# Kernel tuning notes

Hardware: AMD Instinct MI355X
Metric: run time of the kernel (lower is better)

The kernel has to match this reference:

```python
import jax, jax.numpy as jnp
import numpy as np

NU, NI = 100000, 50000          # users, items
N = NU + NI                      # total nodes
E0 = 1200000                     # directed user->item interactions
B = 100000                       # query (user,item) pairs
D = 64                           # embedding_dim
H1, H2, H3 = 128, 128, 64        # hidden_dims


def setup_inputs() -> dict:
    key = jax.random.key(0)
    ks = jax.random.split(key, 20)
    # bipartite edges, made symmetric (as create_graph does)
    u = jax.random.randint(ks[0], (E0,), 0, NU, dtype=jnp.int32)
    it = jax.random.randint(ks[1], (E0,), NU, N, dtype=jnp.int32)
    src = jnp.concatenate([u, it])   # [2*E0]
    dst = jnp.concatenate([it, u])   # [2*E0]
    user_idx = jax.random.randint(ks[2], (B,), 0, NU, dtype=jnp.int32)
    item_idx = jax.random.randint(ks[3], (B,), 0, NI, dtype=jnp.int32)

    def w(k, shape, fan_in):
        return jax.random.normal(k, shape, jnp.float32) * (1.0 / np.sqrt(fan_in))

    return {
        "user_table": jax.random.normal(ks[4], (NU, D), jnp.float32),
        "item_table": jax.random.normal(ks[5], (NI, D), jnp.float32),
        "W1": w(ks[6], (D, H1), D),   "b1": jnp.zeros((H1,), jnp.float32),
        "W2": w(ks[7], (H1, H2), H1), "b2": jnp.zeros((H2,), jnp.float32),
        "W3": w(ks[8], (H2, H3), H2), "b3": jnp.zeros((H3,), jnp.float32),
        "P1": w(ks[9], (2 * H3, 64), 2 * H3), "pb1": jnp.zeros((64,), jnp.float32),
        "P2": w(ks[10], (64, 32), 64),        "pb2": jnp.zeros((32,), jnp.float32),
        "P3": w(ks[11], (32, 1), 32),         "pb3": jnp.zeros((1,), jnp.float32),
        "src": src, "dst": dst,
        "user_idx": user_idx, "item_idx": item_idx,
    }


def _gconv(x, src, dst, deg_rsqrt, W, b):
    # DGL GraphConv, norm='both': D^{-1/2} A D^{-1/2} X W + b
    h = x * deg_rsqrt[:, None]                              # [N, d]
    m = jax.ops.segment_sum(h[src], dst, num_segments=N)    # gather-scatter over edges
    return (m * deg_rsqrt[:, None]) @ W + b


def reference(user_table, item_table, W1, b1, W2, b2, W3, b3,
              P1, pb1, P2, pb2, P3, pb3, src, dst, user_idx, item_idx):
    # symmetric graph -> in-degree == out-degree
    deg = jax.ops.segment_sum(jnp.ones_like(dst, jnp.float32), dst, num_segments=N)
    deg_rsqrt = jax.lax.rsqrt(jnp.maximum(deg, 1.0))

    x = jnp.concatenate([user_table, item_table], axis=0)   # [N, D]
    x = jax.nn.relu(_gconv(x, src, dst, deg_rsqrt, W1, b1))
    x = jax.nn.relu(_gconv(x, src, dst, deg_rsqrt, W2, b2))
    x = _gconv(x, src, dst, deg_rsqrt, W3, b3)               # [N, H3]

    u = x[user_idx]                                          # [B, H3]
    v = x[NU + item_idx]                                     # [B, H3]
    z = jnp.concatenate([u, v], axis=1)                      # [B, 2*H3]
    z = jax.nn.relu(z @ P1 + pb1)
    z = jax.nn.relu(z @ P2 + pb2)
    return jax.nn.sigmoid(z @ P3 + pb3)                      # [B, 1]
```

## Files before the change

kernel.cpp:

```cpp
#include <hip/hip_runtime.h>
#include <hip/hip_bf16.h>


typedef unsigned short u16;
typedef unsigned int   u32;
typedef __attribute__((ext_vector_type(8))) short short8;
typedef __attribute__((ext_vector_type(4))) float f32x4;

__device__ __forceinline__ float b2f(u16 u){
  union { u32 i; float f; } c; c.i = ((u32)u) << 16; return c.f;
}
__device__ __forceinline__ u16 f2b(float f){
  union { float f; u32 i; } c; c.f = f;
  u32 x = c.i;
  u32 r = x + 0x7FFFu + ((x >> 16) & 1u);
  return (u16)(r >> 16);
}

__device__ __forceinline__ void acc8(uint4 u, float* a){
  a[0] += b2f((u16)(u.x & 0xffff)); a[1] += b2f((u16)(u.x >> 16));
  a[2] += b2f((u16)(u.y & 0xffff)); a[3] += b2f((u16)(u.y >> 16));
  a[4] += b2f((u16)(u.z & 0xffff)); a[5] += b2f((u16)(u.z >> 16));
  a[6] += b2f((u16)(u.w & 0xffff)); a[7] += b2f((u16)(u.w >> 16));
}


__global__ __launch_bounds__(256) void k_histK(const int* __restrict__ dst, int ne, int K,
                                               u32* __restrict__ bhist){
  extern __shared__ u32 sh[];
  int t = threadIdx.x;
  for (int i = t; i < K; i += 256) sh[i] = 0;
  __syncthreads();
  for (int i = blockIdx.x*256 + t; i < ne; i += gridDim.x*256)
    atomicAdd(&sh[dst[i] >> 8], 1u);
  __syncthreads();
  int rot = (int)((blockIdx.x * 73u) % (u32)K);
  for (int jj = t; jj < K; jj += 256){
    int i = jj + rot; if (i >= K) i -= K;
    u32 v = sh[i];
    if (v) atomicAdd(&bhist[i], v);
  }
}

__global__ __launch_bounds__(256) void k_scanK(const u32* __restrict__ bhist, int K,
                                               u32* __restrict__ bbase, u32* __restrict__ gcur){
  __shared__ u32 s[256];
  int t = threadIdx.x;
  int items = (K + 255) / 256;
  u32 local[16];
  int s0 = t * items;
  u32 sum = 0;
  for (int j = 0; j < items; j++){
    int idx = s0 + j;
    u32 v = (idx < K) ? bhist[idx] : 0;
    local[j] = v; sum += v;
  }
  s[t] = sum; __syncthreads();
  for (int off = 1; off < 256; off <<= 1){
    u32 add = (t >= off) ? s[t-off] : 0;
    __syncthreads();
    s[t] += add;
    __syncthreads();
  }
  u32 run = s[t] - sum;
  for (int j = 0; j < items; j++){
    int idx = s0 + j;
    if (idx < K){ bbase[idx] = run; gcur[idx] = run; }
    run += local[j];
  }
  if (t == 255) bbase[K] = s[255];
}

__global__ __launch_bounds__(256) void k_scatterR(const int* __restrict__ src, const int* __restrict__ dst,
                                                  int ne, int K, u32* __restrict__ gcur,
                                                  u32* __restrict__ ebuf){
  extern __shared__ u32 cnt[];
  int t = threadIdx.x;
  int e0 = blockIdx.x * 4096;
  for (int i = t; i < K; i += 256) cnt[i] = 0;
  __syncthreads();
#pragma unroll
  for (int j = 0; j < 16; j++){
    int e = e0 + j*256 + t;
    if (e < ne) atomicAdd(&cnt[dst[e] >> 8], 1u);
  }
  __syncthreads();
  int rot = (int)((blockIdx.x * 73u) % (u32)K);
  for (int jj = t; jj < K; jj += 256){
    int i = jj + rot; if (i >= K) i -= K;
    u32 c = cnt[i];
    if (c) cnt[i] = atomicAdd(&gcur[i], c);
  }
  __syncthreads();
#pragma unroll
  for (int j = 0; j < 16; j++){
    int e = e0 + j*256 + t;
    if (e < ne){
      int d = dst[e];
      u32 p = atomicAdd(&cnt[d >> 8], 1u);
      ebuf[p] = ((u32)(d & 255) << 18) | (u32)src[e];
    }
  }
}

__global__ __launch_bounds__(256) void k_csr(const u32* __restrict__ ebuf, const u32* __restrict__ bbase,
                                             int n, int ne, int* __restrict__ row_ptr,
                                             float* __restrict__ r, int* __restrict__ col){
  __shared__ u32 cnt[256];
  __shared__ u32 pfx[256];
  __shared__ u32 cur[256];
  int b = blockIdx.x, t = threadIdx.x;
  u32 bb = bbase[b], be = bbase[b+1];
  int nbase = b << 8;
  int nn = n - nbase; if (nn > 256) nn = 256;
  cnt[t] = 0;
  __syncthreads();
  for (u32 e = bb + t; e < be; e += 256)
    atomicAdd(&cnt[ebuf[e] >> 18], 1u);
  __syncthreads();
  pfx[t] = cnt[t];
  __syncthreads();
  for (int off = 1; off < 256; off <<= 1){
    u32 add = (t >= off) ? pfx[t-off] : 0;
    __syncthreads();
    pfx[t] += add;
    __syncthreads();
  }
  u32 excl = pfx[t] - cnt[t];
  cur[t] = bb + excl;
  if (t < nn){
    row_ptr[nbase + t] = (int)(bb + excl);
    r[nbase + t] = rsqrtf(fmaxf((float)cnt[t], 1.0f));
  }
  __syncthreads();
  for (u32 e = bb + t; e < be; e += 256){
    u32 v = ebuf[e];
    u32 p = atomicAdd(&cur[v >> 18], 1u);
    col[p] = (int)(v & 0x3FFFFu);
  }
  if (b == 0 && t == 0) row_ptr[n] = ne;
}

__global__ __launch_bounds__(256) void k_cvtW(const float* __restrict__ a0, const float* __restrict__ a1,
    const float* __restrict__ a2, const float* __restrict__ a3, const float* __restrict__ a4,
    int n0, int n1, int n2, int n3, int n4, u16* __restrict__ out){
  int i = blockIdx.x*256 + threadIdx.x;
  int idx = i;
  const float* s;
  if (idx < n0){ s = a0; }
  else { idx -= n0;
    if (idx < n1){ s = a1; }
    else { idx -= n1;
      if (idx < n2){ s = a2; }
      else { idx -= n2;
        if (idx < n3){ s = a3; }
        else { idx -= n3;
          if (idx >= n4) return;
          s = a4;
        }
      }
    }
  }
  out[i] = f2b(s[idx]);
}

__global__ __launch_bounds__(256) void k_scale0(const float* __restrict__ ut, const float* __restrict__ it,
    const float* __restrict__ r, u16* __restrict__ x0, int n, int nu){
  int i = blockIdx.x*256 + threadIdx.x;
  int base = i*4;
  if (base < n*64){
    int node = base >> 6;
    float rv = r[node];
    const float* srcp = (node < nu) ? (ut + (size_t)node*64) : (it + (size_t)(node-nu)*64);
    float4 v = *(const float4*)(srcp + (base & 63));
    ushort4 o;
    o.x = f2b(v.x*rv); o.y = f2b(v.y*rv); o.z = f2b(v.z*rv); o.w = f2b(v.w*rv);
    *(ushort4*)(x0 + base) = o;
  }
}

template<int D, bool BIAS>
__global__ __launch_bounds__(256) void k_agg(const u16* __restrict__ x, const float* __restrict__ r,
    const int* __restrict__ row_ptr, const int* __restrict__ col,
    const float* __restrict__ bias, u16* __restrict__ out, int n){
  constexpr int G = D/8;
  constexpr int E = 64/G;
  int wid = (blockIdx.x*256 + threadIdx.x) >> 6;
  int lane = threadIdx.x & 63;
  if (wid >= n) return;
  int gidx = lane / G;
  int l    = lane % G;
  int beg = row_ptr[wid], end = row_ptr[wid+1];
  float a[8] = {0.f,0.f,0.f,0.f,0.f,0.f,0.f,0.f};
  int e = beg + gidx;
  for (; e + E < end; e += 2*E){
    int s0 = col[e];
    int s1 = col[e+E];
    uint4 u0 = *(const uint4*)(x + (size_t)s0*D + l*8);
    uint4 u1 = *(const uint4*)(x + (size_t)s1*D + l*8);
    acc8(u0, a);
    acc8(u1, a);
  }
  if (e < end){
    int s = col[e];
    acc8(*(const uint4*)(x + (size_t)s*D + l*8), a);
  }
#pragma unroll
  for (int off = G; off < 64; off <<= 1){
#pragma unroll
    for (int i = 0; i < 8; i++) a[i] += __shfl_xor(a[i], off);
  }
  if (gidx == 0){
    float rn = r[wid];
    float v[8];
#pragma unroll
    for (int i = 0; i < 8; i++){
      float y = a[i] * rn;
      if constexpr (BIAS) y += bias[l*8 + i];
      v[i] = y;
    }
    uint4 o;
    o.x = (u32)f2b(v[0]) | ((u32)f2b(v[1]) << 16);
    o.y = (u32)f2b(v[2]) | ((u32)f2b(v[3]) << 16);
    o.z = (u32)f2b(v[4]) | ((u32)f2b(v[5]) << 16);
    o.w = (u32)f2b(v[6]) | ((u32)f2b(v[7]) << 16);
    *(uint4*)(out + (size_t)wid*D + l*8) = o;
  }
}

template<int K_, int OUT, bool BIAS, bool RELU, bool SCALE, bool GATHER, bool DOTEP>
__global__ __launch_bounds__(256) void k_mgemm(
    const u16* __restrict__ A, const u16* __restrict__ Wb, const float* __restrict__ bias,
    const float* __restrict__ rr, u16* __restrict__ C, int nrows, int nu,
    const int* __restrict__ uidx, const int* __restrict__ vidx,
    const float* __restrict__ P3, const float* __restrict__ pb3, float* __restrict__ outp)
{
  constexpr int KP = K_ + 8;
  constexpr int NT = OUT / 16;
  constexpr int KS = K_ / 32;
  __shared__ u16 Wt[OUT * KP];
  const int t = threadIdx.x;

  for (int i = t; i < (K_*OUT)/2; i += 256){
    int g = i*2;
    int k = g / OUT, n = g % OUT;
    u32 v = *(const u32*)(Wb + (size_t)k*OUT + n);
    Wt[n*KP + k]     = (u16)(v & 0xffff);
    Wt[(n+1)*KP + k] = (u16)(v >> 16);
  }
  __syncthreads();

  const int wave = t >> 6, lane = t & 63;
  const int quad = lane >> 4, m16 = lane & 15;
  const int rowb = blockIdx.x*128 + wave*32;

  const short8 zz = {0,0,0,0,0,0,0,0};
  short8 afr[2][KS];
#pragma unroll
  for (int mt = 0; mt < 2; mt++){
    int row = rowb + mt*16 + m16;
    bool ok = row < nrows;
#pragma unroll
    for (int ks = 0; ks < KS; ks++){
      int k = ks*32 + quad*8;
      if (!ok){ afr[mt][ks] = zz; continue; }
      if constexpr (GATHER){
        int node, kk;
        if (k < 64){ node = uidx[row];      kk = k; }
        else       { node = nu + vidx[row]; kk = k - 64; }
        afr[mt][ks] = *(const short8*)(A + (size_t)node*64 + kk);
      } else {
        afr[mt][ks] = *(const short8*)(A + (size_t)row*K_ + k);
      }
    }
  }

  f32x4 acc[2][NT];
#pragma unroll
  for (int mt = 0; mt < 2; mt++)
#pragma unroll
    for (int nt = 0; nt < NT; nt++) acc[mt][nt] = (f32x4){0.f,0.f,0.f,0.f};

#pragma unroll
  for (int nt = 0; nt < NT; nt++){
#pragma unroll
    for (int ks = 0; ks < KS; ks++){
      short8 b = *(const short8*)(Wt + (size_t)(nt*16 + m16)*KP + ks*32 + quad*8);
      acc[0][nt] = __builtin_amdgcn_mfma_f32_16x16x32_bf16(afr[0][ks], b, acc[0][nt], 0, 0, 0);
      acc[1][nt] = __builtin_amdgcn_mfma_f32_16x16x32_bf16(afr[1][ks], b, acc[1][nt], 0, 0, 0);
    }
  }

  if constexpr (!DOTEP){
    float bv[NT];
#pragma unroll
    for (int nt = 0; nt < NT; nt++){
      if constexpr (BIAS) bv[nt] = bias[nt*16 + m16]; else bv[nt] = 0.f;
    }
#pragma unroll
    for (int mt = 0; mt < 2; mt++){
      int row0 = rowb + mt*16 + quad*4;
#pragma unroll
      for (int reg = 0; reg < 4; reg++){
        int row = row0 + reg;
        if (row >= nrows) continue;
        float rs = 1.f;
        if constexpr (SCALE) rs = rr[row];
#pragma unroll
        for (int nt = 0; nt < NT; nt++){
          float v = acc[mt][nt][reg];
          if constexpr (BIAS) v += bv[nt];
          if constexpr (RELU) v = fmaxf(v, 0.f);
          if constexpr (SCALE) v *= rs;
          C[(size_t)row*OUT + nt*16 + m16] = f2b(v);
        }
      }
    }
  } else {
    float b0 = bias[m16], b1v = bias[16 + m16];
    float p0 = P3[m16],   p1 = P3[16 + m16];
    float pb = pb3[0];
#pragma unroll
    for (int mt = 0; mt < 2; mt++){
      float v4[4];
#pragma unroll
      for (int reg = 0; reg < 4; reg++){
        float part = fmaxf(acc[mt][0][reg] + b0, 0.f) * p0
                   + fmaxf(acc[mt][1][reg] + b1v, 0.f) * p1;
        part += __shfl_xor(part, 1);
        part += __shfl_xor(part, 2);
        part += __shfl_xor(part, 4);
        part += __shfl_xor(part, 8);
        v4[reg] = 1.f / (1.f + __expf(-(part + pb)));
      }
      if (m16 == 0){
        int row0 = rowb + mt*16 + quad*4;
        if (row0 + 3 < nrows){
          *(float4*)(outp + row0) = make_float4(v4[0], v4[1], v4[2], v4[3]);
        } else {
#pragma unroll
          for (int reg = 0; reg < 4; reg++)
            if (row0 + reg < nrows) outp[row0 + reg] = v4[reg];
        }
      }
    }
  }
}


extern "C" void kernel_launch(void* const* d_in, const int* in_sizes, int n_in,
                              void* d_out, int out_size, void* d_ws, size_t ws_size,
                              hipStream_t stream){
  const float* ut  = (const float*)d_in[0];
  const float* it  = (const float*)d_in[1];
  const float* W1  = (const float*)d_in[2];
  const float* b1  = (const float*)d_in[3];
  const float* W2  = (const float*)d_in[4];
  const float* b2  = (const float*)d_in[5];
  const float* W3  = (const float*)d_in[6];
  const float* b3  = (const float*)d_in[7];
  const float* P1  = (const float*)d_in[8];
  const float* pb1 = (const float*)d_in[9];
  const float* P2  = (const float*)d_in[10];
  const float* pb2 = (const float*)d_in[11];
  const float* P3  = (const float*)d_in[12];
  const float* pb3 = (const float*)d_in[13];
  const int* src  = (const int*)d_in[14];
  const int* dst  = (const int*)d_in[15];
  const int* uidx = (const int*)d_in[16];
  const int* vidx = (const int*)d_in[17];

  const int NU = in_sizes[0] / 64;
  const int NI = in_sizes[1] / 64;
  const int N  = NU + NI;
  const int NE = in_sizes[14];
  const int B  = in_sizes[16];
  const int K  = (N + 255) >> 8;

  char* w = (char*)d_ws;
  auto alloc = [&](size_t bytes)->void*{
    void* p = (void*)w;
    w += (bytes + 255) & ~(size_t)255;
    return p;
  };
  float* r       = (float*)alloc((size_t)N*4);
  int*   row_ptr = (int*)  alloc((size_t)(N+1)*4);
  u32*   bhist   = (u32*)  alloc((size_t)K*4);
  u32*   bbase   = (u32*)  alloc((size_t)(K+1)*4);
  u32*   gcur    = (u32*)  alloc((size_t)K*4);
  int*   col     = (int*)  alloc((size_t)NE*4);
  u16*   Wall    = (u16*)  alloc((size_t)(64*128 + 128*128 + 128*64 + 128*64 + 64*32)*2);
  char*  bufE    = (char*) alloc((size_t)N*64*2 > (size_t)NE*4 ? (size_t)N*64*2 : (size_t)NE*4);
  char*  bufF    = (char*) alloc((size_t)N*128*2);
  u16*   bufC    = (u16*)  alloc((size_t)N*128*2);
  u16*   bufD    = (u16*)  alloc((size_t)N*64*2);
  if ((size_t)(w - (char*)d_ws) > ws_size) return;

  u16* wb1  = Wall;
  u16* wb2  = wb1 + 64*128;
  u16* wb3  = wb2 + 128*128;
  u16* pb1w = wb3 + 128*64;
  u16* pb2w = pb1w + 128*64;
  const int NW = 64*128 + 128*128 + 128*64 + 128*64 + 64*32;

  u32* ebuf = (u32*)bufE;

  hipMemsetAsync(bhist, 0, (size_t)K*4, stream);

  int g;
  k_cvtW   <<<(NW + 255)/256, 256, 0, stream>>>(W1, W2, W3, P1, P2,
              64*128, 128*128, 128*64, 128*64, 64*32, Wall);
  k_histK  <<<128, 256, (size_t)K*4, stream>>>(dst, NE, K, bhist);
  k_scanK  <<<1, 256, 0, stream>>>(bhist, K, bbase, gcur);
  g = (NE + 4095)/4096;
  k_scatterR<<<g, 256, (size_t)K*4, stream>>>(src, dst, NE, K, gcur, ebuf);
  k_csr    <<<K, 256, 0, stream>>>(ebuf, bbase, N, NE, row_ptr, r, col);

  const int ga  = (N + 3)/4;
  const int gN  = (N + 127)/128;
  const int gB  = (B + 127)/128;

  u16* x0 = bufD;
  g = (N*64/4 + 255)/256; k_scale0<<<g,256,0,stream>>>(ut, it, r, x0, N, NU);

  u16* m1 = (u16*)bufE;
  k_agg<64,false><<<ga,256,0,stream>>>(x0, r, row_ptr, col, nullptr, m1, N);
  u16* h1 = bufC;
  k_mgemm<64,128,true,true,true,false,false><<<gN,256,0,stream>>>(
      m1, wb1, b1, r, h1, N, NU, nullptr, nullptr, nullptr, nullptr, nullptr);

  u16* m2 = (u16*)bufF;
  k_agg<128,false><<<ga,256,0,stream>>>(h1, r, row_ptr, col, nullptr, m2, N);
  u16* h2 = bufC;
  k_mgemm<128,128,true,true,true,false,false><<<gN,256,0,stream>>>(
      m2, wb2, b2, r, h2, N, NU, nullptr, nullptr, nullptr, nullptr, nullptr);

  u16* g3 = bufD;
  k_mgemm<128,64,false,false,false,false,false><<<gN,256,0,stream>>>(
      h2, wb3, nullptr, nullptr, g3, N, NU, nullptr, nullptr, nullptr, nullptr, nullptr);

  u16* x3 = (u16*)bufE;
  k_agg<64,true><<<ga,256,0,stream>>>(g3, r, row_ptr, col, b3, x3, N);

  u16* A1 = (u16*)bufF;
  k_mgemm<128,64,true,true,false,true,false><<<gB,256,0,stream>>>(
      x3, pb1w, pb1, nullptr, A1, B, NU, uidx, vidx, nullptr, nullptr, nullptr);

  k_mgemm<64,32,true,true,false,false,true><<<gB,256,0,stream>>>(
      A1, pb2w, pb2, nullptr, nullptr, B, 0, nullptr, nullptr, P3, pb3, (float*)d_out);
}
```

Measured before the change: 488.5 us.

## Fuse weight conversion, input scaling and MLP head; pre-transpose weights

Weight conversion to bf16 moves into the histogram kernel and now writes transposed weights, so the GEMM kernels read B fragments straight from global memory instead of staging a transposed copy in shared memory. The input scaling by degree is folded into the CSR kernel, and the two prediction-head GEMMs are merged into one kernel that keeps the intermediate in shared memory. This removes three launches, one shared-memory transpose per GEMM block and a global round trip of the hidden activations. In exchange, weight fragments are fetched repeatedly from global/L2 instead of shared memory.

```diff
diff --git a/kernel.cpp b/kernel.cpp
--- a/kernel.cpp
+++ b/kernel.cpp
@@ -24,11 +24,24 @@
   a[6] += b2f((u16)(u.w & 0xffff)); a[7] += b2f((u16)(u.w >> 16));
 }
 
+#define NWT 43008
+
 
 __global__ __launch_bounds__(256) void k_histK(const int* __restrict__ dst, int ne, int K,
-                                               u32* __restrict__ bhist){
+    u32* __restrict__ bhist,
+    const float* __restrict__ W1, const float* __restrict__ W2, const float* __restrict__ W3,
+    const float* __restrict__ P1, const float* __restrict__ P2, u16* __restrict__ WT){
   extern __shared__ u32 sh[];
   int t = threadIdx.x;
+  for (int i = blockIdx.x*256 + t; i < NWT; i += gridDim.x*256){
+    float v;
+    if (i < 8192)      { int j=i;        v = W1[(j%64)*128 + j/64];   }
+    else if (i < 24576){ int j=i-8192;   v = W2[(j%128)*128 + j/128]; }
+    else if (i < 32768){ int j=i-24576;  v = W3[(j%128)*64 + j/128];  }
+    else if (i < 40960){ int j=i-32768;  v = P1[(j%128)*64 + j/128];  }
+    else               { int j=i-40960;  v = P2[(j%64)*32 + j/64];    }
+    WT[i] = f2b(v);
+  }
   for (int i = t; i < K; i += 256) sh[i] = 0;
   __syncthreads();
   for (int i = blockIdx.x*256 + t; i < ne; i += gridDim.x*256)
@@ -105,10 +118,13 @@
 
 __global__ __launch_bounds__(256) void k_csr(const u32* __restrict__ ebuf, const u32* __restrict__ bbase,
                                              int n, int ne, int* __restrict__ row_ptr,
-                                             float* __restrict__ r, int* __restrict__ col){
+                                             float* __restrict__ r, int* __restrict__ col,
+                                             const float* __restrict__ ut, const float* __restrict__ it,
+                                             int nu, u16* __restrict__ x0){
   __shared__ u32 cnt[256];
   __shared__ u32 pfx[256];
   __shared__ u32 cur[256];
+  __shared__ float rsh[256];
   int b = blockIdx.x, t = threadIdx.x;
   u32 bb = bbase[b], be = bbase[b+1];
   int nbase = b << 8;
@@ -129,8 +145,10 @@
   u32 excl = pfx[t] - cnt[t];
   cur[t] = bb + excl;
   if (t < nn){
+    float rv = rsqrtf(fmaxf((float)cnt[t], 1.0f));
     row_ptr[nbase + t] = (int)(bb + excl);
-    r[nbase + t] = rsqrtf(fmaxf((float)cnt[t], 1.0f));
+    r[nbase + t] = rv;
+    rsh[t] = rv;
   }
   __syncthreads();
   for (u32 e = bb + t; e < be; e += 256){
@@ -139,43 +157,17 @@
     col[p] = (int)(v & 0x3FFFFu);
   }
   if (b == 0 && t == 0) row_ptr[n] = ne;
-}
-
-__global__ __launch_bounds__(256) void k_cvtW(const float* __restrict__ a0, const float* __restrict__ a1,
-    const float* __restrict__ a2, const float* __restrict__ a3, const float* __restrict__ a4,
-    int n0, int n1, int n2, int n3, int n4, u16* __restrict__ out){
-  int i = blockIdx.x*256 + threadIdx.x;
-  int idx = i;
-  const float* s;
-  if (idx < n0){ s = a0; }
-  else { idx -= n0;
-    if (idx < n1){ s = a1; }
-    else { idx -= n1;
-      if (idx < n2){ s = a2; }
-      else { idx -= n2;
-        if (idx < n3){ s = a3; }
-        else { idx -= n3;
-          if (idx >= n4) return;
-          s = a4;
-        }
-      }
-    }
-  }
-  out[i] = f2b(s[idx]);
-}
-
-__global__ __launch_bounds__(256) void k_scale0(const float* __restrict__ ut, const float* __restrict__ it,
-    const float* __restrict__ r, u16* __restrict__ x0, int n, int nu){
-  int i = blockIdx.x*256 + threadIdx.x;
-  int base = i*4;
-  if (base < n*64){
-    int node = base >> 6;
-    float rv = r[node];
-    const float* srcp = (node < nu) ? (ut + (size_t)node*64) : (it + (size_t)(node-nu)*64);
-    float4 v = *(const float4*)(srcp + (base & 63));
+  for (int i = t; i < nn*16; i += 256){
+    int ln = i >> 4;
+    int node = nbase + ln;
+    int c4 = (i & 15) << 2;
+    float rv = rsh[ln];
+    const float* srcp = (node < nu) ? (ut + (size_t)node*64 + c4)
+                                    : (it + (size_t)(node-nu)*64 + c4);
+    float4 v = *(const float4*)srcp;
     ushort4 o;
     o.x = f2b(v.x*rv); o.y = f2b(v.y*rv); o.z = f2b(v.z*rv); o.w = f2b(v.w*rv);
-    *(ushort4*)(x0 + base) = o;
+    *(ushort4*)(x0 + (size_t)node*64 + c4) = o;
   }
 }
 
@@ -228,28 +220,14 @@
   }
 }
 
-template<int K_, int OUT, bool BIAS, bool RELU, bool SCALE, bool GATHER, bool DOTEP>
+template<int K_, int OUT, bool BIAS, bool RELU, bool SCALE>
 __global__ __launch_bounds__(256) void k_mgemm(
-    const u16* __restrict__ A, const u16* __restrict__ Wb, const float* __restrict__ bias,
-    const float* __restrict__ rr, u16* __restrict__ C, int nrows, int nu,
-    const int* __restrict__ uidx, const int* __restrict__ vidx,
-    const float* __restrict__ P3, const float* __restrict__ pb3, float* __restrict__ outp)
+    const u16* __restrict__ A, const u16* __restrict__ WT, const float* __restrict__ bias,
+    const float* __restrict__ rr, u16* __restrict__ C, int nrows)
 {
-  constexpr int KP = K_ + 8;
   constexpr int NT = OUT / 16;
   constexpr int KS = K_ / 32;
-  __shared__ u16 Wt[OUT * KP];
   const int t = threadIdx.x;
-
-  for (int i = t; i < (K_*OUT)/2; i += 256){
-    int g = i*2;
-    int k = g / OUT, n = g % OUT;
-    u32 v = *(const u32*)(Wb + (size_t)k*OUT + n);
-    Wt[n*KP + k]     = (u16)(v & 0xffff);
-    Wt[(n+1)*KP + k] = (u16)(v >> 16);
-  }
-  __syncthreads();
-
   const int wave = t >> 6, lane = t & 63;
   const int quad = lane >> 4, m16 = lane & 15;
   const int rowb = blockIdx.x*128 + wave*32;
@@ -262,86 +240,158 @@
     bool ok = row < nrows;
 #pragma unroll
     for (int ks = 0; ks < KS; ks++){
+      afr[mt][ks] = ok ? *(const short8*)(A + (size_t)row*K_ + ks*32 + quad*8) : zz;
+    }
+  }
+
+  f32x4 acc[2][NT];
+#pragma unroll
+  for (int mt = 0; mt < 2; mt++)
+#pragma unroll
+    for (int nt = 0; nt < NT; nt++) acc[mt][nt] = (f32x4){0.f,0.f,0.f,0.f};
+
+#pragma unroll
+  for (int nt = 0; nt < NT; nt++){
+#pragma unroll
+    for (int ks = 0; ks < KS; ks++){
+      short8 b = *(const short8*)(WT + (size_t)(nt*16 + m16)*K_ + ks*32 + quad*8);
+      acc[0][nt] = __builtin_amdgcn_mfma_f32_16x16x32_bf16(afr[0][ks], b, acc[0][nt], 0, 0, 0);
+      acc[1][nt] = __builtin_amdgcn_mfma_f32_16x16x32_bf16(afr[1][ks], b, acc[1][nt], 0, 0, 0);
+    }
+  }
+
+  float bv[NT];
+#pragma unroll
+  for (int nt = 0; nt < NT; nt++){
+    if constexpr (BIAS) bv[nt] = bias[nt*16 + m16]; else bv[nt] = 0.f;
+  }
+#pragma unroll
+  for (int mt = 0; mt < 2; mt++){
+    int row0 = rowb + mt*16 + quad*4;
+#pragma unroll
+    for (int reg = 0; reg < 4; reg++){
+      int row = row0 + reg;
+      if (row >= nrows) continue;
+      float rs = 1.f;
+      if constexpr (SCALE) rs = rr[row];
+#pragma unroll
+      for (int nt = 0; nt < NT; nt++){
+        float v = acc[mt][nt][reg];
+        if constexpr (BIAS) v += bv[nt];
+        if constexpr (RELU) v = fmaxf(v, 0.f);
+        if constexpr (SCALE) v *= rs;
+        C[(size_t)row*OUT + nt*16 + m16] = f2b(v);
+      }
+    }
+  }
+}
+
+__global__ __launch_bounds__(256) void k_mlp(
+    const u16* __restrict__ x3, const u16* __restrict__ WT4, const float* __restrict__ pb1v,
+    const u16* __restrict__ WT5, const float* __restrict__ pb2v,
+    const float* __restrict__ P3, const float* __restrict__ pb3,
+    const int* __restrict__ uidx, const int* __restrict__ vidx,
+    int B, int nu, float* __restrict__ outp)
+{
+  __shared__ u16 a1[128*72];
+  const int t = threadIdx.x;
+  const int wave = t >> 6, lane = t & 63;
+  const int quad = lane >> 4, m16 = lane & 15;
+  const int rowb = blockIdx.x*128 + wave*32;
+
+  const short8 zz = {0,0,0,0,0,0,0,0};
+  short8 afr[2][4];
+#pragma unroll
+  for (int mt = 0; mt < 2; mt++){
+    int row = rowb + mt*16 + m16;
+    bool ok = row < B;
+#pragma unroll
+    for (int ks = 0; ks < 4; ks++){
       int k = ks*32 + quad*8;
       if (!ok){ afr[mt][ks] = zz; continue; }
-      if constexpr (GATHER){
-        int node, kk;
-        if (k < 64){ node = uidx[row];      kk = k; }
-        else       { node = nu + vidx[row]; kk = k - 64; }
-        afr[mt][ks] = *(const short8*)(A + (size_t)node*64 + kk);
-      } else {
-        afr[mt][ks] = *(const short8*)(A + (size_t)row*K_ + k);
-      }
-    }
-  }
-
-  f32x4 acc[2][NT];
+      int node, kk;
+      if (k < 64){ node = uidx[row];      kk = k; }
+      else       { node = nu + vidx[row]; kk = k - 64; }
+      afr[mt][ks] = *(const short8*)(x3 + (size_t)node*64 + kk);
+    }
+  }
+  f32x4 acc[2][4];
 #pragma unroll
   for (int mt = 0; mt < 2; mt++)
 #pragma unroll
-    for (int nt = 0; nt < NT; nt++) acc[mt][nt] = (f32x4){0.f,0.f,0.f,0.f};
-
-#pragma unroll
-  for (int nt = 0; nt < NT; nt++){
-#pragma unroll
-    for (int ks = 0; ks < KS; ks++){
-      short8 b = *(const short8*)(Wt + (size_t)(nt*16 + m16)*KP + ks*32 + quad*8);
+    for (int nt = 0; nt < 4; nt++) acc[mt][nt] = (f32x4){0.f,0.f,0.f,0.f};
+#pragma unroll
+  for (int nt = 0; nt < 4; nt++){
+#pragma unroll
+    for (int ks = 0; ks < 4; ks++){
+      short8 b = *(const short8*)(WT4 + (size_t)(nt*16 + m16)*128 + ks*32 + quad*8);
       acc[0][nt] = __builtin_amdgcn_mfma_f32_16x16x32_bf16(afr[0][ks], b, acc[0][nt], 0, 0, 0);
       acc[1][nt] = __builtin_amdgcn_mfma_f32_16x16x32_bf16(afr[1][ks], b, acc[1][nt], 0, 0, 0);
     }
   }
-
-  if constexpr (!DOTEP){
-    float bv[NT];
-#pragma unroll
-    for (int nt = 0; nt < NT; nt++){
-      if constexpr (BIAS) bv[nt] = bias[nt*16 + m16]; else bv[nt] = 0.f;
-    }
-#pragma unroll
-    for (int mt = 0; mt < 2; mt++){
+  float pb1s[4];
+#pragma unroll
+  for (int nt = 0; nt < 4; nt++) pb1s[nt] = pb1v[nt*16 + m16];
+#pragma unroll
+  for (int mt = 0; mt < 2; mt++){
+    int rl0 = wave*32 + mt*16 + quad*4;
+#pragma unroll
+    for (int reg = 0; reg < 4; reg++){
+#pragma unroll
+      for (int nt = 0; nt < 4; nt++){
+        float v = fmaxf(acc[mt][nt][reg] + pb1s[nt], 0.f);
+        a1[(rl0 + reg)*72 + nt*16 + m16] = f2b(v);
+      }
+    }
+  }
+  __syncthreads();
+
+  short8 af2[2][2];
+#pragma unroll
+  for (int mt = 0; mt < 2; mt++){
+    int rl = wave*32 + mt*16 + m16;
+#pragma unroll
+    for (int ks = 0; ks < 2; ks++)
+      af2[mt][ks] = *(const short8*)(a1 + rl*72 + ks*32 + quad*8);
+  }
+  f32x4 acc2[2][2];
+#pragma unroll
+  for (int mt = 0; mt < 2; mt++)
+#pragma unroll
+    for (int nt = 0; nt < 2; nt++) acc2[mt][nt] = (f32x4){0.f,0.f,0.f,0.f};
+#pragma unroll
+  for (int nt = 0; nt < 2; nt++){
+#pragma unroll
+    for (int ks = 0; ks < 2; ks++){
+      short8 b = *(const short8*)(WT5 + (size_t)(nt*16 + m16)*64 + ks*32 + quad*8);
+      acc2[0][nt] = __builtin_amdgcn_mfma_f32_16x16x32_bf16(af2[0][ks], b, acc2[0][nt], 0, 0, 0);
+      acc2[1][nt] = __builtin_amdgcn_mfma_f32_16x16x32_bf16(af2[1][ks], b, acc2[1][nt], 0, 0, 0);
+    }
+  }
+  float b0 = pb2v[m16], b1v = pb2v[16 + m16];
+  float p0 = P3[m16],   p1 = P3[16 + m16];
+  float pb = pb3[0];
+#pragma unroll
+  for (int mt = 0; mt < 2; mt++){
+    float v4[4];
+#pragma unroll
+    for (int reg = 0; reg < 4; reg++){
+      float part = fmaxf(acc2[mt][0][reg] + b0, 0.f) * p0
+                 + fmaxf(acc2[mt][1][reg] + b1v, 0.f) * p1;
+      part += __shfl_xor(part, 1);
+      part += __shfl_xor(part, 2);
+      part += __shfl_xor(part, 4);
+      part += __shfl_xor(part, 8);
+      v4[reg] = 1.f / (1.f + __expf(-(part + pb)));
+    }
+    if (m16 == 0){
       int row0 = rowb + mt*16 + quad*4;
-#pragma unroll
-      for (int reg = 0; reg < 4; reg++){
-        int row = row0 + reg;
-        if (row >= nrows) continue;
-        float rs = 1.f;
-        if constexpr (SCALE) rs = rr[row];
-#pragma unroll
-        for (int nt = 0; nt < NT; nt++){
-          float v = acc[mt][nt][reg];
-          if constexpr (BIAS) v += bv[nt];
-          if constexpr (RELU) v = fmaxf(v, 0.f);
-          if constexpr (SCALE) v *= rs;
-          C[(size_t)row*OUT + nt*16 + m16] = f2b(v);
-        }
-      }
-    }
-  } else {
-    float b0 = bias[m16], b1v = bias[16 + m16];
-    float p0 = P3[m16],   p1 = P3[16 + m16];
-    float pb = pb3[0];
-#pragma unroll
-    for (int mt = 0; mt < 2; mt++){
-      float v4[4];
-#pragma unroll
-      for (int reg = 0; reg < 4; reg++){
-        float part = fmaxf(acc[mt][0][reg] + b0, 0.f) * p0
-                   + fmaxf(acc[mt][1][reg] + b1v, 0.f) * p1;
-        part += __shfl_xor(part, 1);
-        part += __shfl_xor(part, 2);
-        part += __shfl_xor(part, 4);
-        part += __shfl_xor(part, 8);
-        v4[reg] = 1.f / (1.f + __expf(-(part + pb)));
-      }
-      if (m16 == 0){
-        int row0 = rowb + mt*16 + quad*4;
-        if (row0 + 3 < nrows){
-          *(float4*)(outp + row0) = make_float4(v4[0], v4[1], v4[2], v4[3]);
-        } else {
-#pragma unroll
-          for (int reg = 0; reg < 4; reg++)
-            if (row0 + reg < nrows) outp[row0 + reg] = v4[reg];
-        }
+      if (row0 + 3 < B){
+        *(float4*)(outp + row0) = make_float4(v4[0], v4[1], v4[2], v4[3]);
+      } else {
+#pragma unroll
+        for (int reg = 0; reg < 4; reg++)
+          if (row0 + reg < B) outp[row0 + reg] = v4[reg];
       }
     }
   }
@@ -389,63 +439,50 @@
   u32*   bbase   = (u32*)  alloc((size_t)(K+1)*4);
   u32*   gcur    = (u32*)  alloc((size_t)K*4);
   int*   col     = (int*)  alloc((size_t)NE*4);
-  u16*   Wall    = (u16*)  alloc((size_t)(64*128 + 128*128 + 128*64 + 128*64 + 64*32)*2);
+  u16*   Wall    = (u16*)  alloc((size_t)NWT*2);
   char*  bufE    = (char*) alloc((size_t)N*64*2 > (size_t)NE*4 ? (size_t)N*64*2 : (size_t)NE*4);
   char*  bufF    = (char*) alloc((size_t)N*128*2);
   u16*   bufC    = (u16*)  alloc((size_t)N*128*2);
   u16*   bufD    = (u16*)  alloc((size_t)N*64*2);
   if ((size_t)(w - (char*)d_ws) > ws_size) return;
 
-  u16* wb1  = Wall;
-  u16* wb2  = wb1 + 64*128;
-  u16* wb3  = wb2 + 128*128;
-  u16* pb1w = wb3 + 128*64;
-  u16* pb2w = pb1w + 128*64;
-  const int NW = 64*128 + 128*128 + 128*64 + 128*64 + 64*32;
+  u16* WT1 = Wall;
+  u16* WT2 = Wall + 8192;
+  u16* WT3 = Wall + 24576;
+  u16* WT4 = Wall + 32768;
+  u16* WT5 = Wall + 40960;
 
   u32* ebuf = (u32*)bufE;
+  u16* x0   = bufD;
 
   hipMemsetAsync(bhist, 0, (size_t)K*4, stream);
 
   int g;
-  k_cvtW   <<<(NW + 255)/256, 256, 0, stream>>>(W1, W2, W3, P1, P2,
-              64*128, 128*128, 128*64, 128*64, 64*32, Wall);
-  k_histK  <<<128, 256, (size_t)K*4, stream>>>(dst, NE, K, bhist);
+  k_histK  <<<128, 256, (size_t)K*4, stream>>>(dst, NE, K, bhist, W1, W2, W3, P1, P2, Wall);
   k_scanK  <<<1, 256, 0, stream>>>(bhist, K, bbase, gcur);
   g = (NE + 4095)/4096;
   k_scatterR<<<g, 256, (size_t)K*4, stream>>>(src, dst, NE, K, gcur, ebuf);
-  k_csr    <<<K, 256, 0, stream>>>(ebuf, bbase, N, NE, row_ptr, r, col);
+  k_csr    <<<K, 256, 0, stream>>>(ebuf, bbase, N, NE, row_ptr, r, col, ut, it, NU, x0);
 
   const int ga  = (N + 3)/4;
   const int gN  = (N + 127)/128;
   const int gB  = (B + 127)/128;
 
-  u16* x0 = bufD;
-  g = (N*64/4 + 255)/256; k_scale0<<<g,256,0,stream>>>(ut, it, r, x0, N, NU);
-
   u16* m1 = (u16*)bufE;
   k_agg<64,false><<<ga,256,0,stream>>>(x0, r, row_ptr, col, nullptr, m1, N);
   u16* h1 = bufC;
-  k_mgemm<64,128,true,true,true,false,false><<<gN,256,0,stream>>>(
-      m1, wb1, b1, r, h1, N, NU, nullptr, nullptr, nullptr, nullptr, nullptr);
+  k_mgemm<64,128,true,true,true><<<gN,256,0,stream>>>(m1, WT1, b1, r, h1, N);
 
   u16* m2 = (u16*)bufF;
   k_agg<128,false><<<ga,256,0,stream>>>(h1, r, row_ptr, col, nullptr, m2, N);
   u16* h2 = bufC;
-  k_mgemm<128,128,true,true,true,false,false><<<gN,256,0,stream>>>(
-      m2, wb2, b2, r, h2, N, NU, nullptr, nullptr, nullptr, nullptr, nullptr);
+  k_mgemm<128,128,true,true,true><<<gN,256,0,stream>>>(m2, WT2, b2, r, h2, N);
 
   u16* g3 = bufD;
-  k_mgemm<128,64,false,false,false,false,false><<<gN,256,0,stream>>>(
-      h2, wb3, nullptr, nullptr, g3, N, NU, nullptr, nullptr, nullptr, nullptr, nullptr);
+  k_mgemm<128,64,false,false,false><<<gN,256,0,stream>>>(h2, WT3, nullptr, nullptr, g3, N);
 
   u16* x3 = (u16*)bufE;
   k_agg<64,true><<<ga,256,0,stream>>>(g3, r, row_ptr, col, b3, x3, N);
 
-  u16* A1 = (u16*)bufF;
-  k_mgemm<128,64,true,true,false,true,false><<<gB,256,0,stream>>>(
-      x3, pb1w, pb1, nullptr, A1, B, NU, uidx, vidx, nullptr, nullptr, nullptr);
-
-  k_mgemm<64,32,true,true,false,false,true><<<gB,256,0,stream>>>(
-      A1, pb2w, pb2, nullptr, nullptr, B, 0, nullptr, nullptr, P3, pb3, (float*)d_out);
-}
+  k_mlp<<<gB,256,0,stream>>>(x3, WT4, pb1, WT5, pb2, P3, pb3, uidx, vidx, B, NU, (float*)d_out);
+}
```

New measurement: 510.3 us. 4.5% more time.
